# Optimization experiments

Measured on AMD Instinct MI355X. Metric: run time of the kernel, lower is better.

Reference implementation:

```python
import jax, jax.numpy as jnp
import numpy as np

N = 2048; C_IN = 2; H = 32; EMB = 16; OUT = 1; HORIZON = 12
B = 32; T = 16

def setup_inputs() -> dict:
    key = jax.random.key(0)
    ks = jax.random.split(key, 10)
    s = 0.05
    return {
        "x":  jax.random.normal(ks[0], (B, T, N, C_IN), dtype=jnp.float32),
        "E1": jax.random.normal(ks[1], (N, EMB), dtype=jnp.float32) * 0.1,
        "E2": jax.random.normal(ks[2], (N, EMB), dtype=jnp.float32) * 0.1,
        "Wx": jax.random.normal(ks[3], (C_IN, 4 * H), dtype=jnp.float32) * s,
        "bx": jnp.zeros((4 * H,), dtype=jnp.float32),
        "Wh": jax.random.normal(ks[4], (H, 4 * H), dtype=jnp.float32) * s,
        "bh": jnp.zeros((4 * H,), dtype=jnp.float32),
        "Wp": jax.random.normal(ks[5], (H, OUT * HORIZON), dtype=jnp.float32) * s,
        "bp": jnp.zeros((OUT * HORIZON,), dtype=jnp.float32),
    }

def reference(x, E1, E2, Wx, bx, Wh, bh, Wp, bp):
    Bb, Tt, Nn, _ = x.shape
    # adaptive adjacency: softmax(relu(E1 @ E2^T)) over last dim  [N,N]
    A = jax.nn.softmax(jax.nn.relu(E1 @ E2.T), axis=-1)

    def step(carry, xt):
        h, c = carry  # [B,N,H]
        # fused graph-conv gates: (A @ xt) Wx + (A @ h) Wh + biases -> [B,N,4H]
        gates = (jnp.einsum('ij,bjc->bic', A, xt) @ Wx + bx
                 + jnp.einsum('ij,bjh->bih', A, h) @ Wh + bh)
        i, f, o, g = jnp.split(gates, 4, axis=-1)
        i = jax.nn.sigmoid(i); f = jax.nn.sigmoid(f); o = jax.nn.sigmoid(o)
        g = jnp.tanh(g)
        c_t = f * c + i * g
        h_t = o * jnp.tanh(c_t)
        return (h_t, c_t), None

    h0 = jnp.zeros((Bb, Nn, H), dtype=x.dtype)
    c0 = jnp.zeros((Bb, Nn, H), dtype=x.dtype)
    (h_last, _), _ = jax.lax.scan(step, (h0, c0), jnp.transpose(x, (1, 0, 2, 3)))
    out = h_last @ Wp + bp                      # [B,N,horizon*out]
    out = out.reshape(Bb, Nn, HORIZON, OUT)
    return jnp.transpose(out, (0, 2, 1, 3))     # [B,horizon,N,out]
```

## Files before the change

### kernel.cpp

```cpp
#include <hip/hip_runtime.h>
#include <hip/hip_bf16.h>
#include <cstddef>
#include <cstdint>

#define NN 2048
#define CIN 2
#define HH 32
#define EMB 16
#define HOR 12
#define BB 32
#define TT 16
#define GC 128
#define XCOLS 1024
#define HCOLS 1024

#define ATILE_STRIDE 65536
#define BTILE_STRIDE 32768
#define LOPLANE 2097152

typedef __attribute__((ext_vector_type(8))) _Float16 f16x8;
typedef __attribute__((ext_vector_type(16))) float f32x16;

__device__ __forceinline__ void load_lds16(const void* g, void* l) {
    __builtin_amdgcn_global_load_lds(
        (const __attribute__((address_space(1))) void*)g,
        (__attribute__((address_space(3))) void*)l, 16, 0, 0);
}

__global__ __launch_bounds__(256) void e2_transpose(const float* __restrict__ E2,
                                                    float* __restrict__ E2T) {
    const int idx = blockIdx.x * 256 + threadIdx.x;
    const int k = idx >> 11;
    const int j = idx & 2047;
    E2T[idx] = E2[j * EMB + k];
}

__global__ __launch_bounds__(256) void precompute(const float* __restrict__ E1,
                                                  const float* __restrict__ E2T,
                                                  const float* __restrict__ x,
                                                  const float* __restrict__ Wx,
                                                  const float* __restrict__ bx,
                                                  const float* __restrict__ Wh,
                                                  const float* __restrict__ bh,
                                                  _Float16* __restrict__ A2,
                                                  _Float16* __restrict__ B2x,
                                                  _Float16* __restrict__ W16,
                                                  float* __restrict__ Wxr,
                                                  float* __restrict__ bfold) {
    const int blk = blockIdx.x;
    const int tid = threadIdx.x;

    if (blk < 512) {
        const int i = blk * 4 + (tid >> 6);
        const int l = tid & 63;
        float e1[EMB];
#pragma unroll
        for (int k = 0; k < EMB; ++k) e1[k] = E1[i * EMB + k];

        float s[32];
#pragma unroll
        for (int c = 0; c < 32; ++c) s[c] = 0.f;
#pragma unroll
        for (int k = 0; k < EMB; ++k) {
            const float ek = e1[k];
            const float* p = E2T + k * 2048 + l;
#pragma unroll
            for (int c = 0; c < 32; ++c) s[c] = fmaf(ek, p[c * 64], s[c]);
        }
        float mx = 0.f;
#pragma unroll
        for (int c = 0; c < 32; ++c) { s[c] = fmaxf(s[c], 0.f); mx = fmaxf(mx, s[c]); }
#pragma unroll
        for (int off = 32; off > 0; off >>= 1) mx = fmaxf(mx, __shfl_xor(mx, off, 64));
        float sum = 0.f;
#pragma unroll
        for (int c = 0; c < 32; ++c) { s[c] = expf(s[c] - mx); sum += s[c]; }
#pragma unroll
        for (int off = 32; off > 0; off >>= 1) sum += __shfl_xor(sum, off, 64);
        const float inv = 1.0f / sum;
        const int chb = (l >> 3);
        const int e   = l & 7;
#pragma unroll
        for (int c = 0; c < 32; ++c)
            A2[((size_t)(c * 8 + chb) * 2048 + i) * 8 + e] = (_Float16)(s[c] * inv);
    } else if (blk < 512 + 1024) {
        const int idx = (blk - 512) * 256 + tid;
        const int col = idx & 1023;
        const int jc  = idx >> 10;
        const int bt  = col >> 1;
        const int c   = col & 1;
        const float* xp = x + ((size_t)bt * NN + jc * 8) * CIN + c;
        f16x8 vh, vl;
#pragma unroll
        for (int e = 0; e < 8; ++e) {
            const float v = xp[e * CIN];
            const _Float16 hi = (_Float16)v;
            vh[e] = hi;
            vl[e] = (_Float16)(v - (float)hi);
        }
        const size_t base = ((size_t)jc * 1024 + col) * 8;
        *(f16x8*)(B2x + base) = vh;
        *(f16x8*)(B2x + base + LOPLANE) = vl;
    } else {
#pragma unroll
        for (int r = 0; r < 32; ++r) {
            const int idx = r * 256 + tid;
            const int e  = idx & 7;
            const int ln = (idx >> 3) & 63;
            const int gq = (idx >> 9) & 3;
            const int kh = (idx >> 11) & 1;
            const int k  = kh * 16 + (ln >> 5) * 8 + e;
            const int ch = gq * 32 + (ln & 31);
            const float v = Wh[k * GC + (ch & 3) * HH + (ch >> 2)];
            const _Float16 hi = (_Float16)v;
            W16[idx] = hi;
            W16[8192 + idx] = (_Float16)(v - (float)hi);
        }
        {
            const int idx = tid;
            const int c = idx >> 7, rem = idx & 127;
            const int h = rem >> 2, g = rem & 3;
            Wxr[idx] = Wx[c * GC + g * HH + h];
        }
        if (tid < 128) {
            const int h = tid >> 2, g = tid & 3;
            bfold[tid] = bx[g * HH + h] + bh[g * HH + h];
        }
    }
}

template <int NPROD, int GATE>
__global__ __launch_bounds__(512, 2) void gemm_fused(const _Float16* __restrict__ A2,
                                                     const _Float16* __restrict__ B2,
                                                     float* __restrict__ Cout,
                                                     const float* __restrict__ AX,
                                                     const _Float16* __restrict__ W16,
                                                     const float* __restrict__ Wxr,
                                                     const float* __restrict__ bfold,
                                                     float* __restrict__ cst,
                                                     float* __restrict__ h32,
                                                     _Float16* __restrict__ hTout,
                                                     int t, int last) {
    constexpr int SUBS   = (NPROD == 1) ? 2 : 1;
    constexpr int NT     = 64 / SUBS;
    constexpr int SUBBUF = 4096 + NPROD * 8192;
    constexpr int BUF    = SUBS * SUBBUF;
    constexpr int NBUF   = (NPROD == 1) ? 4 : 6;
    constexpr int PCH    = 256 + NPROD * 512;
    constexpr int NG     = (SUBS * PCH) / 64;
    constexpr int GMAX   = 3;
    constexpr int STAGE_SZ = NBUF * BUF;
    constexpr int SMEMSZ = GATE ? (STAGE_SZ + 1024 + 512 + 2048) : STAGE_SZ;
    __shared__ __align__(16) char smem[SMEMSZ];

    const int tid  = threadIdx.x;
    const int w    = tid >> 6;
    const int lane = tid & 63;

    const int wg = blockIdx.x;
    const int x8 = wg & 7;
    const int s  = wg >> 3;
    const int mb = (x8 >> 1) * 8 + (s & 7);
    const int nb = (x8 & 1) * 4 + (s >> 3);
    const int m0 = mb * 64;
    const int n0 = nb * 128;

    float* wxr_s = nullptr; float* bfl_s = nullptr; float* axs = nullptr;
    if constexpr (GATE) {
        wxr_s = (float*)(smem + STAGE_SZ);
        bfl_s = (float*)(smem + STAGE_SZ + 1024);
        axs   = (float*)(smem + STAGE_SZ + 1536);
        const int b0c = nb * 4;
        if (tid < 64) *(float4*)&wxr_s[tid * 4] = *(const float4*)&Wxr[tid * 4];
        if (tid < 32) *(float4*)&bfl_s[tid * 4] = *(const float4*)&bfold[tid * 4];
        axs[tid] = AX[(size_t)(m0 + (tid & 63)) * XCOLS +
                      ((b0c + (tid >> 7)) * TT + t) * CIN + ((tid >> 6) & 1)];
    }

    const _Float16* gp[GMAX];
    int lbase[GMAX];
    int adv[GMAX];
    bool val[GMAX];
#pragma unroll
    for (int i = 0; i < GMAX; ++i) {
        const int g = w + 8 * i;
        val[i] = (g < NG);
        const int gg = val[i] ? g : 0;
        const int cid  = gg * 64 + lane;
        const int cid0 = gg * 64;
        const int su  = cid / PCH,  r  = cid  - su * PCH;
        const int su0 = cid0 / PCH, r0 = cid0 - su0 * PCH;
        if (r < 256) {
            gp[i]  = A2 + ((size_t)((su * 4 + (r >> 6)) * 2048) + m0 + (r & 63)) * 8;
            adv[i] = SUBS * ATILE_STRIDE;
        } else {
            const int r2 = r - 256;
            gp[i]  = B2 + (size_t)(r2 >> 9) * LOPLANE
                        + ((size_t)((su * 4 + ((r2 & 511) >> 7)) * 1024) + n0 + (r2 & 127)) * 8;
            adv[i] = SUBS * BTILE_STRIDE;
        }
        lbase[i] = su0 * SUBBUF + (r0 < 256 ? r0 * 16 : 4096 + (r0 - 256) * 16);
    }

    const int lrow = lane & 31, lg = lane >> 5;
    const int mi = w >> 2;
    const int gq = w & 3;
    const int wc = gq * 32;
    const int aoff0 = lg * 1024 + (mi * 32 + lrow) * 16;
    const int aoff1 = 2048 + lg * 1024 + (mi * 32 + lrow) * 16;
    const int boff0 = 4096 + lg * 2048 + (wc + lrow) * 16;
    const int boff1 = 4096 + 4096 + lg * 2048 + (wc + lrow) * 16;

    f32x16 acc0 = (f32x16)(0.0f), acc1 = (f32x16)(0.0f);

#define STAGE(BUFI) do {                                                       \
    char* lb = smem + (BUFI) * BUF;                                            \
    _Pragma("unroll")                                                          \
    for (int i = 0; i < GMAX; ++i) if (val[i]) {                               \
        load_lds16(gp[i], lb + lbase[i]);                                      \
        gp[i] += adv[i];                                                       \
    }                                                                          \
} while (0)

#define VMW(NHI, NLO) do {                                                     \
    if (w < 4) asm volatile("s_waitcnt vmcnt(" #NHI ")" ::: "memory");         \
    else       asm volatile("s_waitcnt vmcnt(" #NLO ")" ::: "memory");         \
} while (0)

#define BAR() do {                                                             \
    __builtin_amdgcn_s_barrier();                                              \
    asm volatile("" ::: "memory");                                             \
} while (0)

#define COMPUTE(BUFI) do {                                                     \
    const char* sb = smem + (BUFI) * BUF;                                      \
    _Pragma("unroll")                                                          \
    for (int su = 0; su < SUBS; ++su) {                                        \
        const char* st = sb + su * SUBBUF;                                     \
        f16x8 fa0 = *(const f16x8*)(st + aoff0);                               \
        f16x8 fa1 = *(const f16x8*)(st + aoff1);                               \
        f16x8 fb0 = *(const f16x8*)(st + boff0);                               \
        f16x8 fb1 = *(const f16x8*)(st + boff1);                               \
        acc0 = __builtin_amdgcn_mfma_f32_32x32x16_f16(fa0, fb0, acc0, 0, 0, 0);\
        acc1 = __builtin_amdgcn_mfma_f32_32x32x16_f16(fa1, fb1, acc1, 0, 0, 0);\
        if constexpr (NPROD == 2) {                                            \
            f16x8 fc0 = *(const f16x8*)(st + boff0 + 8192);                    \
            f16x8 fc1 = *(const f16x8*)(st + boff1 + 8192);                    \
            acc0 = __builtin_amdgcn_mfma_f32_32x32x16_f16(fa0, fc0, acc0, 0, 0, 0); \
            acc1 = __builtin_amdgcn_mfma_f32_32x32x16_f16(fa1, fc1, acc1, 0, 0, 0); \
        }                                                                      \
    }                                                                          \
} while (0)

    if constexpr (NPROD == 1) {
        STAGE(0);
        STAGE(1);
#pragma unroll 1
        for (int it = 0; it < NT - 2; ++it) {
            STAGE((it + 2) & 3);
            asm volatile("s_waitcnt vmcnt(6)" ::: "memory");
            BAR();
            COMPUTE(it & 3);
        }
        asm volatile("s_waitcnt vmcnt(3)" ::: "memory");
        BAR();
        COMPUTE((NT - 2) & 3);
        asm volatile("s_waitcnt vmcnt(0)" ::: "memory");
        BAR();
        COMPUTE((NT - 1) & 3);
    } else {
        STAGE(0);
        STAGE(1);
        STAGE(2);
        int bs = 3, bc = 0;
#pragma unroll 1
        for (int it = 0; it < NT - 3; ++it) {
            STAGE(bs);
            VMW(9, 6);
            BAR();
            COMPUTE(bc);
            bs = (bs == 5) ? 0 : bs + 1;
            bc = (bc == 5) ? 0 : bc + 1;
        }
        VMW(6, 4);
        BAR();
        COMPUTE(bc); bc = (bc == 5) ? 0 : bc + 1;
        VMW(3, 2);
        BAR();
        COMPUTE(bc); bc = (bc == 5) ? 0 : bc + 1;
        asm volatile("s_waitcnt vmcnt(0)" ::: "memory");
        BAR();
        COMPUTE(bc);
    }
#undef STAGE
#undef VMW
#undef BAR
#undef COMPUTE

    if constexpr (!GATE) {
        const int colg = n0 + wc + lrow;
#pragma unroll
        for (int r = 0; r < 16; ++r) {
            const int rp = (r & 3) + 8 * (r >> 2) + 4 * lg;
            Cout[(size_t)(m0 + mi * 32 + rp) * XCOLS + colg] = acc0[r] + acc1[r];
        }
    } else {
        f16x8 wbh0 = *(const f16x8*)(W16 + ((size_t)(0 * 4 + gq) * 64 + lane) * 8);
        f16x8 wbh1 = *(const f16x8*)(W16 + ((size_t)(1 * 4 + gq) * 64 + lane) * 8);
        f16x8 wbl0 = *(const f16x8*)(W16 + 8192 + ((size_t)(0 * 4 + gq) * 64 + lane) * 8);
        f16x8 wbl1 = *(const f16x8*)(W16 + 8192 + ((size_t)(1 * 4 + gq) * 64 + lane) * 8);

        _Float16* ahh = (_Float16*)smem;
        _Float16* ahl = (_Float16*)(smem + 17408);
        const int colw = wc + lrow;
#pragma unroll
        for (int r = 0; r < 16; ++r) {
            const int rp = (r & 3) + 8 * (r >> 2) + 4 * lg;
            const float v = acc0[r] + acc1[r];
            const _Float16 hi = (_Float16)v;
            ahh[(mi * 32 + rp) * 136 + colw] = hi;
            ahl[(mi * 32 + rp) * 136 + colw] = (_Float16)(v - (float)hi);
        }
        __syncthreads();

        f32x16 g0 = (f32x16)(0.0f), g1 = (f32x16)(0.0f);
        f32x16 g2 = (f32x16)(0.0f), g3 = (f32x16)(0.0f);
#define GATEB(ACC, b) do {                                                         \
    const int arow = (mi * 32 + lrow) * 136 + (b) * 32 + lg * 8;                   \
    f16x8 fh0 = *(const f16x8*)(ahh + arow);                                       \
    f16x8 fl0 = *(const f16x8*)(ahl + arow);                                       \
    f16x8 fh1 = *(const f16x8*)(ahh + arow + 16);                                  \
    f16x8 fl1 = *(const f16x8*)(ahl + arow + 16);                                  \
    ACC = __builtin_amdgcn_mfma_f32_32x32x16_f16(fh0, wbh0, ACC, 0, 0, 0);         \
    ACC = __builtin_amdgcn_mfma_f32_32x32x16_f16(fh0, wbl0, ACC, 0, 0, 0);         \
    ACC = __builtin_amdgcn_mfma_f32_32x32x16_f16(fl0, wbh0, ACC, 0, 0, 0);         \
    ACC = __builtin_amdgcn_mfma_f32_32x32x16_f16(fh1, wbh1, ACC, 0, 0, 0);         \
    ACC = __builtin_amdgcn_mfma_f32_32x32x16_f16(fh1, wbl1, ACC, 0, 0, 0);         \
    ACC = __builtin_amdgcn_mfma_f32_32x32x16_f16(fl1, wbh1, ACC, 0, 0, 0);         \
} while (0)
        GATEB(g0, 0); GATEB(g1, 1); GATEB(g2, 2); GATEB(g3, 3);
#undef GATEB

        float* gl = (float*)(smem + 34816);
        const int nl2 = tid & 63;
        const int hb  = (tid >> 6) * 4;
        const int b0c = nb * 4;
        const int nd  = m0 + nl2;
        const size_t ntbase = ((size_t)((nd >> 5) * 4 + ((nd >> 3) & 3)) * 1024) * 8 + (nd & 7);

#define POINT(ACC, bi) do {                                                        \
    _Pragma("unroll")                                                              \
    for (int r = 0; r < 16; ++r) {                                                 \
        const int rp = (r & 3) + 8 * (r >> 2) + 4 * lg;                            \
        gl[(mi * 32 + rp) * 132 + gq * 32 + lrow] = ACC[r];                        \
    }                                                                              \
    __syncthreads();                                                               \
    {                                                                              \
        const float ax0 = axs[(bi) * 128 + nl2];                                   \
        const float ax1 = axs[(bi) * 128 + 64 + nl2];                              \
        const int bb = b0c + (bi);                                                 \
        const size_t off = (size_t)nd * HCOLS + bb * HH + hb;                      \
        const float4 co = *(const float4*)(cst + off);                             \
        const float cold[4] = {co.x, co.y, co.z, co.w};                            \
        float cn[4], hn[4];                                                        \
        _Pragma("unroll")                                                          \
        for (int p = 0; p < 4; ++p) {                                              \
            const int hh = hb + p;                                                 \
            const float4 gt = *(const float4*)(gl + nl2 * 132 + hh * 4);           \
            const float a0 = gt.x + bfl_s[hh*4+0] + ax0*wxr_s[hh*4+0] + ax1*wxr_s[128+hh*4+0]; \
            const float a1 = gt.y + bfl_s[hh*4+1] + ax0*wxr_s[hh*4+1] + ax1*wxr_s[128+hh*4+1]; \
            const float a2 = gt.z + bfl_s[hh*4+2] + ax0*wxr_s[hh*4+2] + ax1*wxr_s[128+hh*4+2]; \
            const float a3 = gt.w + bfl_s[hh*4+3] + ax0*wxr_s[hh*4+3] + ax1*wxr_s[128+hh*4+3]; \
            const float i_ = 1.0f / (1.0f + expf(-a0));                            \
            const float f_ = 1.0f / (1.0f + expf(-a1));                            \
            const float o_ = 1.0f / (1.0f + expf(-a2));                            \
            const float g_ = tanhf(a3);                                            \
            const float ct = f_ * cold[p] + i_ * g_;                               \
            cn[p] = ct;                                                            \
            hn[p] = o_ * tanhf(ct);                                                \
        }                                                                          \
        *(float4*)(cst + off) = make_float4(cn[0], cn[1], cn[2], cn[3]);           \
        if (last) *(float4*)(h32 + off) = make_float4(hn[0], hn[1], hn[2], hn[3]); \
        _Pragma("unroll")                                                          \
        for (int p = 0; p < 4; ++p)                                                \
            hTout[ntbase + (size_t)(bb * HH + hb + p) * 8] = (_Float16)hn[p];      \
    }                                                                              \
    __syncthreads();                                                               \
} while (0)
        POINT(g0, 0); POINT(g1, 1); POINT(g2, 2); POINT(g3, 3);
#undef POINT
    }
}

__global__ __launch_bounds__(256) void gate_update(const float* __restrict__ AX,
                                                   const float* __restrict__ Wxr,
                                                   const float* __restrict__ bfold,
                                                   float* __restrict__ c,
                                                   float* __restrict__ h32,
                                                   _Float16* __restrict__ hT) {
    const int n0 = blockIdx.x * 64;
    const int b0 = blockIdx.y * 4;
    const int tid = threadIdx.x;
    __shared__ float wxr[256];
    __shared__ float bfl[128];
    __shared__ float axs[2][64];

    if (tid < 64)  *(float4*)&wxr[tid * 4] = *(const float4*)&Wxr[tid * 4];
    if (tid < 32)  *(float4*)&bfl[tid * 4] = *(const float4*)&bfold[tid * 4];

    const int nl = tid & 63;
    const int hq = tid >> 6;

    const int nd = n0 + nl;
    const size_t ntbase = ((size_t)((nd >> 5) * 4 + ((nd >> 3) & 3)) * 1024) * 8 + (nd & 7);

#pragma unroll 1
    for (int bi = 0; bi < 4; ++bi) {
        const int b = b0 + bi;
        if (bi) __syncthreads();
        if (tid < 128) {
            const int which = tid >> 6, nls = tid & 63;
            axs[which][nls] = AX[(size_t)(n0 + nls) * XCOLS + (b * TT + 0) * CIN + which];
        }
        __syncthreads();

        const float ax0 = axs[0][nl], ax1 = axs[1][nl];
        float cn[8], hn[8];
#pragma unroll
        for (int u = 0; u < 8; ++u) {
            const int h = hq * 8 + u;
            float a0 = bfl[h * 4 + 0] + ax0 * wxr[h * 4 + 0] + ax1 * wxr[128 + h * 4 + 0];
            float a1 = bfl[h * 4 + 1] + ax0 * wxr[h * 4 + 1] + ax1 * wxr[128 + h * 4 + 1];
            float a2 = bfl[h * 4 + 2] + ax0 * wxr[h * 4 + 2] + ax1 * wxr[128 + h * 4 + 2];
            float a3 = bfl[h * 4 + 3] + ax0 * wxr[h * 4 + 3] + ax1 * wxr[128 + h * 4 + 3];
            const float i_ = 1.0f / (1.0f + expf(-a0));
            const float f_ = 1.0f / (1.0f + expf(-a1));
            const float o_ = 1.0f / (1.0f + expf(-a2));
            const float g_ = tanhf(a3);
            const float ct = i_ * g_;
            (void)f_;
            cn[u] = ct;
            hn[u] = o_ * tanhf(ct);
        }
        const size_t off = (size_t)nd * HCOLS + b * HH + hq * 8;
        *(float4*)(c + off)       = make_float4(cn[0], cn[1], cn[2], cn[3]);
        *(float4*)(c + off + 4)   = make_float4(cn[4], cn[5], cn[6], cn[7]);
        *(float4*)(h32 + off)     = make_float4(hn[0], hn[1], hn[2], hn[3]);
        *(float4*)(h32 + off + 4) = make_float4(hn[4], hn[5], hn[6], hn[7]);
#pragma unroll
        for (int u = 0; u < 8; ++u)
            hT[ntbase + (size_t)(b * HH + hq * 8 + u) * 8] = (_Float16)hn[u];
    }
}

__global__ __launch_bounds__(256) void head_kernel(const float* __restrict__ h,
                                                   const float* __restrict__ Wp,
                                                   const float* __restrict__ bp,
                                                   float* __restrict__ out) {
    const int idx = blockIdx.x * 256 + threadIdx.x;
    const int b = idx >> 11;
    const int n = idx & (NN - 1);
    float hv[HH];
    const float* hp = h + (size_t)n * HCOLS + b * HH;
#pragma unroll
    for (int k = 0; k < HH; ++k) hv[k] = hp[k];
#pragma unroll
    for (int th = 0; th < HOR; ++th) {
        float acc = bp[th];
#pragma unroll
        for (int k = 0; k < HH; ++k) acc += hv[k] * Wp[k * HOR + th];
        out[((size_t)b * HOR + th) * NN + n] = acc;
    }
}

extern "C" void kernel_launch(void* const* d_in, const int* in_sizes, int n_in,
                              void* d_out, int out_size, void* d_ws, size_t ws_size,
                              hipStream_t stream) {
    const float* x  = (const float*)d_in[0];
    const float* E1 = (const float*)d_in[1];
    const float* E2 = (const float*)d_in[2];
    const float* Wx = (const float*)d_in[3];
    const float* bx = (const float*)d_in[4];
    const float* Wh = (const float*)d_in[5];
    const float* bh = (const float*)d_in[6];
    const float* Wp = (const float*)d_in[7];
    const float* bp = (const float*)d_in[8];

    char* ws = (char*)d_ws;
    _Float16* A2  = (_Float16*)(ws);
    _Float16* B2x = (_Float16*)(ws + ( 8ull << 20));
    _Float16* hT0 = (_Float16*)(ws + (16ull << 20));
    _Float16* hT1 = (_Float16*)(ws + (20ull << 20));
    float* AX   = (float*)(ws + (24ull << 20));
    float* cst  = (float*)(ws + (32ull << 20));
    float* h32  = (float*)(ws + (40ull << 20));
    float* Wxr  = (float*)(ws + (48ull << 20) + 65536);
    float* bfold= (float*)(ws + (48ull << 20) + 131072);
    _Float16* W16 = (_Float16*)(ws + (48ull << 20) + 262144);
    float* E2T  = (float*)(ws + (48ull << 20) + 524288);
    _Float16* hTb[2] = {hT0, hT1};

    e2_transpose<<<128, 256, 0, stream>>>(E2, E2T);

    precompute<<<512 + 1024 + 1, 256, 0, stream>>>(E1, E2T, x, Wx, bx, Wh, bh,
                                                   A2, B2x, W16, Wxr, bfold);

    gemm_fused<2, 0><<<256, 512, 0, stream>>>(A2, B2x, AX, nullptr, nullptr, nullptr,
                                              nullptr, nullptr, nullptr, nullptr, 0, 0);

    gate_update<<<dim3(NN / 64, BB / 4), 256, 0, stream>>>(AX, Wxr, bfold,
                                                           cst, h32, hTb[0]);
    for (int t = 1; t < TT; ++t) {
        gemm_fused<1, 1><<<256, 512, 0, stream>>>(A2, hTb[(t + 1) & 1], nullptr, AX,
                                                  W16, Wxr, bfold, cst, h32,
                                                  hTb[t & 1], t, t == TT - 1 ? 1 : 0);
    }

    head_kernel<<<(BB * NN) / 256, 256, 0, stream>>>(h32, Wp, bp, (float*)d_out);
}
```

Measured before the change: 531.1 us.

## Split K across two wave groups in 1024-thread gemm_fused with LDS reduction

Doubles the workgroup to 1024 threads. The two groups of 8 waves each compute half of the K work: one sub-buffer in the recurrent GEMM, one B plane in the input GEMM. The partial accumulators are then reduced through LDS. The gate epilogue is also split so each half handles two of the four batch gates, and the staging loads and waitcnt thresholds are adjusted to match. This aims to raise wave-level parallelism and MFMA throughput per CU, at the cost of an extra LDS reduction, extra barriers and occupancy limited to one workgroup per CU.

```diff
diff --git a/kernel.cpp b/kernel.cpp
--- a/kernel.cpp
+++ b/kernel.cpp
@@ -130,17 +130,17 @@
 }
 
 template <int NPROD, int GATE>
-__global__ __launch_bounds__(512, 2) void gemm_fused(const _Float16* __restrict__ A2,
-                                                     const _Float16* __restrict__ B2,
-                                                     float* __restrict__ Cout,
-                                                     const float* __restrict__ AX,
-                                                     const _Float16* __restrict__ W16,
-                                                     const float* __restrict__ Wxr,
-                                                     const float* __restrict__ bfold,
-                                                     float* __restrict__ cst,
-                                                     float* __restrict__ h32,
-                                                     _Float16* __restrict__ hTout,
-                                                     int t, int last) {
+__global__ __launch_bounds__(1024, 1) void gemm_fused(const _Float16* __restrict__ A2,
+                                                      const _Float16* __restrict__ B2,
+                                                      float* __restrict__ Cout,
+                                                      const float* __restrict__ AX,
+                                                      const _Float16* __restrict__ W16,
+                                                      const float* __restrict__ Wxr,
+                                                      const float* __restrict__ bfold,
+                                                      float* __restrict__ cst,
+                                                      float* __restrict__ h32,
+                                                      _Float16* __restrict__ hTout,
+                                                      int t, int last) {
     constexpr int SUBS   = (NPROD == 1) ? 2 : 1;
     constexpr int NT     = 64 / SUBS;
     constexpr int SUBBUF = 4096 + NPROD * 8192;
@@ -148,14 +148,17 @@
     constexpr int NBUF   = (NPROD == 1) ? 4 : 6;
     constexpr int PCH    = 256 + NPROD * 512;
     constexpr int NG     = (SUBS * PCH) / 64;
-    constexpr int GMAX   = 3;
+    constexpr int GMAX   = 2;
     constexpr int STAGE_SZ = NBUF * BUF;
-    constexpr int SMEMSZ = GATE ? (STAGE_SZ + 1024 + 512 + 2048) : STAGE_SZ;
+    constexpr int REDOFF = (NPROD == 1) ? 34816 : 86016;
+    constexpr int SMEMSZ = GATE ? 105984 : STAGE_SZ;
     __shared__ __align__(16) char smem[SMEMSZ];
 
     const int tid  = threadIdx.x;
     const int w    = tid >> 6;
     const int lane = tid & 63;
+    const int ws   = w & 7;
+    const int kv   = w >> 3;
 
     const int wg = blockIdx.x;
     const int x8 = wg & 7;
@@ -167,14 +170,15 @@
 
     float* wxr_s = nullptr; float* bfl_s = nullptr; float* axs = nullptr;
     if constexpr (GATE) {
-        wxr_s = (float*)(smem + STAGE_SZ);
-        bfl_s = (float*)(smem + STAGE_SZ + 1024);
-        axs   = (float*)(smem + STAGE_SZ + 1536);
+        wxr_s = (float*)(smem + 102400);
+        bfl_s = (float*)(smem + 103424);
+        axs   = (float*)(smem + 103936);
         const int b0c = nb * 4;
         if (tid < 64) *(float4*)&wxr_s[tid * 4] = *(const float4*)&Wxr[tid * 4];
-        if (tid < 32) *(float4*)&bfl_s[tid * 4] = *(const float4*)&bfold[tid * 4];
-        axs[tid] = AX[(size_t)(m0 + (tid & 63)) * XCOLS +
-                      ((b0c + (tid >> 7)) * TT + t) * CIN + ((tid >> 6) & 1)];
+        if (tid >= 64 && tid < 96) *(float4*)&bfl_s[(tid - 64) * 4] = *(const float4*)&bfold[(tid - 64) * 4];
+        if (tid < 512)
+            axs[tid] = AX[(size_t)(m0 + (tid & 63)) * XCOLS +
+                          ((b0c + (tid >> 7)) * TT + t) * CIN + ((tid >> 6) & 1)];
     }
 
     const _Float16* gp[GMAX];
@@ -183,7 +187,7 @@
     bool val[GMAX];
 #pragma unroll
     for (int i = 0; i < GMAX; ++i) {
-        const int g = w + 8 * i;
+        const int g = w + 16 * i;
         val[i] = (g < NG);
         const int gg = val[i] ? g : 0;
         const int cid  = gg * 64 + lane;
@@ -203,13 +207,15 @@
     }
 
     const int lrow = lane & 31, lg = lane >> 5;
-    const int mi = w >> 2;
-    const int gq = w & 3;
+    const int mi = ws >> 2;
+    const int gq = ws & 3;
     const int wc = gq * 32;
-    const int aoff0 = lg * 1024 + (mi * 32 + lrow) * 16;
-    const int aoff1 = 2048 + lg * 1024 + (mi * 32 + lrow) * 16;
-    const int boff0 = 4096 + lg * 2048 + (wc + lrow) * 16;
-    const int boff1 = 4096 + 4096 + lg * 2048 + (wc + lrow) * 16;
+    const int subbase = (NPROD == 1) ? kv * SUBBUF : 0;
+    const int aoff0 = subbase + lg * 1024 + (mi * 32 + lrow) * 16;
+    const int aoff1 = subbase + 2048 + lg * 1024 + (mi * 32 + lrow) * 16;
+    const int bplane = (NPROD == 2) ? kv * 8192 : 0;
+    const int boff0 = subbase + 4096 + bplane + lg * 2048 + (wc + lrow) * 16;
+    const int boff1 = subbase + 4096 + bplane + 4096 + lg * 2048 + (wc + lrow) * 16;
 
     f32x16 acc0 = (f32x16)(0.0f), acc1 = (f32x16)(0.0f);
 
@@ -222,9 +228,9 @@
     }                                                                          \
 } while (0)
 
-#define VMW(NHI, NLO) do {                                                     \
-    if (w < 4) asm volatile("s_waitcnt vmcnt(" #NHI ")" ::: "memory");         \
-    else       asm volatile("s_waitcnt vmcnt(" #NLO ")" ::: "memory");         \
+#define VMW(PRED, NHI, NLO) do {                                               \
+    if (PRED) asm volatile("s_waitcnt vmcnt(" #NHI ")" ::: "memory");          \
+    else      asm volatile("s_waitcnt vmcnt(" #NLO ")" ::: "memory");          \
 } while (0)
 
 #define BAR() do {                                                             \
@@ -233,23 +239,13 @@
 } while (0)
 
 #define COMPUTE(BUFI) do {                                                     \
-    const char* sb = smem + (BUFI) * BUF;                                      \
-    _Pragma("unroll")                                                          \
-    for (int su = 0; su < SUBS; ++su) {                                        \
-        const char* st = sb + su * SUBBUF;                                     \
-        f16x8 fa0 = *(const f16x8*)(st + aoff0);                               \
-        f16x8 fa1 = *(const f16x8*)(st + aoff1);                               \
-        f16x8 fb0 = *(const f16x8*)(st + boff0);                               \
-        f16x8 fb1 = *(const f16x8*)(st + boff1);                               \
-        acc0 = __builtin_amdgcn_mfma_f32_32x32x16_f16(fa0, fb0, acc0, 0, 0, 0);\
-        acc1 = __builtin_amdgcn_mfma_f32_32x32x16_f16(fa1, fb1, acc1, 0, 0, 0);\
-        if constexpr (NPROD == 2) {                                            \
-            f16x8 fc0 = *(const f16x8*)(st + boff0 + 8192);                    \
-            f16x8 fc1 = *(const f16x8*)(st + boff1 + 8192);                    \
-            acc0 = __builtin_amdgcn_mfma_f32_32x32x16_f16(fa0, fc0, acc0, 0, 0, 0); \
-            acc1 = __builtin_amdgcn_mfma_f32_32x32x16_f16(fa1, fc1, acc1, 0, 0, 0); \
-        }                                                                      \
-    }                                                                          \
+    const char* st = smem + (BUFI) * BUF;                                      \
+    f16x8 fa0 = *(const f16x8*)(st + aoff0);                                   \
+    f16x8 fa1 = *(const f16x8*)(st + aoff1);                                   \
+    f16x8 fb0 = *(const f16x8*)(st + boff0);                                   \
+    f16x8 fb1 = *(const f16x8*)(st + boff1);                                   \
+    acc0 = __builtin_amdgcn_mfma_f32_32x32x16_f16(fa0, fb0, acc0, 0, 0, 0);    \
+    acc1 = __builtin_amdgcn_mfma_f32_32x32x16_f16(fa1, fb1, acc1, 0, 0, 0);    \
 } while (0)
 
     if constexpr (NPROD == 1) {
@@ -258,11 +254,11 @@
 #pragma unroll 1
         for (int it = 0; it < NT - 2; ++it) {
             STAGE((it + 2) & 3);
-            asm volatile("s_waitcnt vmcnt(6)" ::: "memory");
+            VMW(w < 8, 4, 2);
             BAR();
             COMPUTE(it & 3);
         }
-        asm volatile("s_waitcnt vmcnt(3)" ::: "memory");
+        VMW(w < 8, 2, 1);
         BAR();
         COMPUTE((NT - 2) & 3);
         asm volatile("s_waitcnt vmcnt(0)" ::: "memory");
@@ -276,16 +272,16 @@
 #pragma unroll 1
         for (int it = 0; it < NT - 3; ++it) {
             STAGE(bs);
-            VMW(9, 6);
+            VMW(w < 4, 6, 3);
             BAR();
             COMPUTE(bc);
             bs = (bs == 5) ? 0 : bs + 1;
             bc = (bc == 5) ? 0 : bc + 1;
         }
-        VMW(6, 4);
+        VMW(w < 4, 4, 2);
         BAR();
         COMPUTE(bc); bc = (bc == 5) ? 0 : bc + 1;
-        VMW(3, 2);
+        VMW(w < 4, 2, 1);
         BAR();
         COMPUTE(bc); bc = (bc == 5) ? 0 : bc + 1;
         asm volatile("s_waitcnt vmcnt(0)" ::: "memory");
@@ -297,12 +293,32 @@
 #undef BAR
 #undef COMPUTE
 
+    f32x16 fin;
+#pragma unroll
+    for (int r = 0; r < 16; ++r) fin[r] = acc0[r] + acc1[r];
+    {
+        float* red = (float*)(smem + REDOFF);
+        if (kv == 1) {
+            float* rp = red + ws * 1024 + lane;
+#pragma unroll
+            for (int r = 0; r < 16; ++r) rp[r * 64] = fin[r];
+        }
+        __syncthreads();
+        if (kv == 0) {
+            const float* rp = red + ws * 1024 + lane;
+#pragma unroll
+            for (int r = 0; r < 16; ++r) fin[r] += rp[r * 64];
+        }
+    }
+
     if constexpr (!GATE) {
-        const int colg = n0 + wc + lrow;
-#pragma unroll
-        for (int r = 0; r < 16; ++r) {
-            const int rp = (r & 3) + 8 * (r >> 2) + 4 * lg;
-            Cout[(size_t)(m0 + mi * 32 + rp) * XCOLS + colg] = acc0[r] + acc1[r];
+        if (kv == 0) {
+            const int colg = n0 + wc + lrow;
+#pragma unroll
+            for (int r = 0; r < 16; ++r) {
+                const int rp = (r & 3) + 8 * (r >> 2) + 4 * lg;
+                Cout[(size_t)(m0 + mi * 32 + rp) * XCOLS + colg] = fin[r];
+            }
         }
     } else {
         f16x8 wbh0 = *(const f16x8*)(W16 + ((size_t)(0 * 4 + gq) * 64 + lane) * 8);
@@ -312,19 +328,20 @@
 
         _Float16* ahh = (_Float16*)smem;
         _Float16* ahl = (_Float16*)(smem + 17408);
-        const int colw = wc + lrow;
-#pragma unroll
-        for (int r = 0; r < 16; ++r) {
-            const int rp = (r & 3) + 8 * (r >> 2) + 4 * lg;
-            const float v = acc0[r] + acc1[r];
-            const _Float16 hi = (_Float16)v;
-            ahh[(mi * 32 + rp) * 136 + colw] = hi;
-            ahl[(mi * 32 + rp) * 136 + colw] = (_Float16)(v - (float)hi);
+        if (kv == 0) {
+            const int colw = wc + lrow;
+#pragma unroll
+            for (int r = 0; r < 16; ++r) {
+                const int rp = (r & 3) + 8 * (r >> 2) + 4 * lg;
+                const float v = fin[r];
+                const _Float16 hi = (_Float16)v;
+                ahh[(mi * 32 + rp) * 136 + colw] = hi;
+                ahl[(mi * 32 + rp) * 136 + colw] = (_Float16)(v - (float)hi);
+            }
         }
         __syncthreads();
 
         f32x16 g0 = (f32x16)(0.0f), g1 = (f32x16)(0.0f);
-        f32x16 g2 = (f32x16)(0.0f), g3 = (f32x16)(0.0f);
 #define GATEB(ACC, b) do {                                                         \
     const int arow = (mi * 32 + lrow) * 136 + (b) * 32 + lg * 8;                   \
     f16x8 fh0 = *(const f16x8*)(ahh + arow);                                       \
@@ -338,27 +355,32 @@
     ACC = __builtin_amdgcn_mfma_f32_32x32x16_f16(fh1, wbl1, ACC, 0, 0, 0);         \
     ACC = __builtin_amdgcn_mfma_f32_32x32x16_f16(fl1, wbh1, ACC, 0, 0, 0);         \
 } while (0)
-        GATEB(g0, 0); GATEB(g1, 1); GATEB(g2, 2); GATEB(g3, 3);
+        GATEB(g0, kv * 2 + 0);
+        GATEB(g1, kv * 2 + 1);
 #undef GATEB
 
-        float* gl = (float*)(smem + 34816);
-        const int nl2 = tid & 63;
-        const int hb  = (tid >> 6) * 4;
+        float* glk = (float*)(smem + 34816 + kv * 33792);
+        const int kvt  = tid >> 9;
+        const int tid2 = tid & 511;
+        float* glt = (float*)(smem + 34816 + kvt * 33792);
+        const int nl2 = tid2 & 63;
+        const int hb  = (tid2 >> 6) * 4;
         const int b0c = nb * 4;
         const int nd  = m0 + nl2;
         const size_t ntbase = ((size_t)((nd >> 5) * 4 + ((nd >> 3) & 3)) * 1024) * 8 + (nd & 7);
 
-#define POINT(ACC, bi) do {                                                        \
+#define POINTR(GACC, R) do {                                                       \
     _Pragma("unroll")                                                              \
     for (int r = 0; r < 16; ++r) {                                                 \
         const int rp = (r & 3) + 8 * (r >> 2) + 4 * lg;                            \
-        gl[(mi * 32 + rp) * 132 + gq * 32 + lrow] = ACC[r];                        \
+        glk[(mi * 32 + rp) * 132 + gq * 32 + lrow] = GACC[r];                      \
     }                                                                              \
     __syncthreads();                                                               \
     {                                                                              \
-        const float ax0 = axs[(bi) * 128 + nl2];                                   \
-        const float ax1 = axs[(bi) * 128 + 64 + nl2];                              \
-        const int bb = b0c + (bi);                                                 \
+        const int bl  = kvt * 2 + (R);                       \
+        const float ax0 = axs[bl * 128 + nl2];                                     \
+        const float ax1 = axs[bl * 128 + 64 + nl2];                                \
+        const int bb = b0c + bl;                                                   \
         const size_t off = (size_t)nd * HCOLS + bb * HH + hb;                      \
         const float4 co = *(const float4*)(cst + off);                             \
         const float cold[4] = {co.x, co.y, co.z, co.w};                            \
@@ -366,7 +388,7 @@
         _Pragma("unroll")                                                          \
         for (int p = 0; p < 4; ++p) {                                              \
             const int hh = hb + p;                                                 \
-            const float4 gt = *(const float4*)(gl + nl2 * 132 + hh * 4);           \
+            const float4 gt = *(const float4*)(glt + nl2 * 132 + hh * 4);          \
             const float a0 = gt.x + bfl_s[hh*4+0] + ax0*wxr_s[hh*4+0] + ax1*wxr_s[128+hh*4+0]; \
             const float a1 = gt.y + bfl_s[hh*4+1] + ax0*wxr_s[hh*4+1] + ax1*wxr_s[128+hh*4+1]; \
             const float a2 = gt.z + bfl_s[hh*4+2] + ax0*wxr_s[hh*4+2] + ax1*wxr_s[128+hh*4+2]; \
@@ -387,8 +409,9 @@
     }                                                                              \
     __syncthreads();                                                               \
 } while (0)
-        POINT(g0, 0); POINT(g1, 1); POINT(g2, 2); POINT(g3, 3);
-#undef POINT
+        POINTR(g0, 0);
+        POINTR(g1, 1);
+#undef POINTR
     }
 }
 
@@ -505,15 +528,15 @@
     precompute<<<512 + 1024 + 1, 256, 0, stream>>>(E1, E2T, x, Wx, bx, Wh, bh,
                                                    A2, B2x, W16, Wxr, bfold);
 
-    gemm_fused<2, 0><<<256, 512, 0, stream>>>(A2, B2x, AX, nullptr, nullptr, nullptr,
-                                              nullptr, nullptr, nullptr, nullptr, 0, 0);
+    gemm_fused<2, 0><<<256, 1024, 0, stream>>>(A2, B2x, AX, nullptr, nullptr, nullptr,
+                                               nullptr, nullptr, nullptr, nullptr, 0, 0);
 
     gate_update<<<dim3(NN / 64, BB / 4), 256, 0, stream>>>(AX, Wxr, bfold,
                                                            cst, h32, hTb[0]);
     for (int t = 1; t < TT; ++t) {
-        gemm_fused<1, 1><<<256, 512, 0, stream>>>(A2, hTb[(t + 1) & 1], nullptr, AX,
-                                                  W16, Wxr, bfold, cst, h32,
-                                                  hTb[t & 1], t, t == TT - 1 ? 1 : 0);
+        gemm_fused<1, 1><<<256, 1024, 0, stream>>>(A2, hTb[(t + 1) & 1], nullptr, AX,
+                                                   W16, Wxr, bfold, cst, h32,
+                                                   hTb[t & 1], t, t == TT - 1 ? 1 : 0);
     }
 
     head_kernel<<<(BB * NN) / 256, 256, 0, stream>>>(h32, Wp, bp, (float*)d_out);
```

Result: no change. 533.6 us (+0.5%).

## Split K across wave pairs in single-product GEMM path with LDS reduction

Applied to the files above, without the earlier changes.

For the NPROD==1 path, each wave now covers both 32-row M tiles and handles one K sub-slice, where before each wave covered one M tile and looped over all sub-slices. Partial accumulators from the two K-halves are summed through LDS before the epilogue. Each B fragment load now feeds two MFMAs, which cuts LDS reads per MFMA. The cost is extra accumulator registers, an LDS reduction with two additional barriers, and the epilogue running on only half the waves.

```diff
diff --git a/kernel.cpp b/kernel.cpp
--- a/kernel.cpp
+++ b/kernel.cpp
@@ -210,8 +210,18 @@
     const int aoff1 = 2048 + lg * 1024 + (mi * 32 + lrow) * 16;
     const int boff0 = 4096 + lg * 2048 + (wc + lrow) * 16;
     const int boff1 = 4096 + 4096 + lg * 2048 + (wc + lrow) * 16;
+    const int gqk = w & 3;
+    const int kvk = w >> 2;
+    const int subb  = kvk * SUBBUF;
+    const int a00 = subb + lg * 1024 + lrow * 16;
+    const int a01 = subb + 2048 + lg * 1024 + lrow * 16;
+    const int a10 = a00 + 512;
+    const int a11 = a01 + 512;
+    const int bk0 = subb + 4096 + lg * 2048 + (gqk * 32 + lrow) * 16;
+    const int bk1 = bk0 + 4096;
 
     f32x16 acc0 = (f32x16)(0.0f), acc1 = (f32x16)(0.0f);
+    f32x16 acc2 = (f32x16)(0.0f), acc3 = (f32x16)(0.0f);
 
 #define STAGE(BUFI) do {                                                       \
     char* lb = smem + (BUFI) * BUF;                                            \
@@ -232,24 +242,32 @@
     asm volatile("" ::: "memory");                                             \
 } while (0)
 
-#define COMPUTE(BUFI) do {                                                     \
-    const char* sb = smem + (BUFI) * BUF;                                      \
-    _Pragma("unroll")                                                          \
-    for (int su = 0; su < SUBS; ++su) {                                        \
-        const char* st = sb + su * SUBBUF;                                     \
-        f16x8 fa0 = *(const f16x8*)(st + aoff0);                               \
-        f16x8 fa1 = *(const f16x8*)(st + aoff1);                               \
-        f16x8 fb0 = *(const f16x8*)(st + boff0);                               \
-        f16x8 fb1 = *(const f16x8*)(st + boff1);                               \
-        acc0 = __builtin_amdgcn_mfma_f32_32x32x16_f16(fa0, fb0, acc0, 0, 0, 0);\
-        acc1 = __builtin_amdgcn_mfma_f32_32x32x16_f16(fa1, fb1, acc1, 0, 0, 0);\
-        if constexpr (NPROD == 2) {                                            \
-            f16x8 fc0 = *(const f16x8*)(st + boff0 + 8192);                    \
-            f16x8 fc1 = *(const f16x8*)(st + boff1 + 8192);                    \
-            acc0 = __builtin_amdgcn_mfma_f32_32x32x16_f16(fa0, fc0, acc0, 0, 0, 0); \
-            acc1 = __builtin_amdgcn_mfma_f32_32x32x16_f16(fa1, fc1, acc1, 0, 0, 0); \
-        }                                                                      \
-    }                                                                          \
+#define COMPUTE1(BUFI) do {                                                    \
+    const char* st = smem + (BUFI) * BUF;                                      \
+    f16x8 fa00 = *(const f16x8*)(st + a00);                                    \
+    f16x8 fa01 = *(const f16x8*)(st + a01);                                    \
+    f16x8 fa10 = *(const f16x8*)(st + a10);                                    \
+    f16x8 fa11 = *(const f16x8*)(st + a11);                                    \
+    f16x8 fb0  = *(const f16x8*)(st + bk0);                                    \
+    f16x8 fb1  = *(const f16x8*)(st + bk1);                                    \
+    acc0 = __builtin_amdgcn_mfma_f32_32x32x16_f16(fa00, fb0, acc0, 0, 0, 0);   \
+    acc1 = __builtin_amdgcn_mfma_f32_32x32x16_f16(fa01, fb1, acc1, 0, 0, 0);   \
+    acc2 = __builtin_amdgcn_mfma_f32_32x32x16_f16(fa10, fb0, acc2, 0, 0, 0);   \
+    acc3 = __builtin_amdgcn_mfma_f32_32x32x16_f16(fa11, fb1, acc3, 0, 0, 0);   \
+} while (0)
+
+#define COMPUTE2(BUFI) do {                                                    \
+    const char* st = smem + (BUFI) * BUF;                                      \
+    f16x8 fa0 = *(const f16x8*)(st + aoff0);                                   \
+    f16x8 fa1 = *(const f16x8*)(st + aoff1);                                   \
+    f16x8 fb0 = *(const f16x8*)(st + boff0);                                   \
+    f16x8 fb1 = *(const f16x8*)(st + boff1);                                   \
+    acc0 = __builtin_amdgcn_mfma_f32_32x32x16_f16(fa0, fb0, acc0, 0, 0, 0);    \
+    acc1 = __builtin_amdgcn_mfma_f32_32x32x16_f16(fa1, fb1, acc1, 0, 0, 0);    \
+    f16x8 fc0 = *(const f16x8*)(st + boff0 + 8192);                            \
+    f16x8 fc1 = *(const f16x8*)(st + boff1 + 8192);                            \
+    acc0 = __builtin_amdgcn_mfma_f32_32x32x16_f16(fa0, fc0, acc0, 0, 0, 0);    \
+    acc1 = __builtin_amdgcn_mfma_f32_32x32x16_f16(fa1, fc1, acc1, 0, 0, 0);    \
 } while (0)
 
     if constexpr (NPROD == 1) {
@@ -260,14 +278,14 @@
             STAGE((it + 2) & 3);
             asm volatile("s_waitcnt vmcnt(6)" ::: "memory");
             BAR();
-            COMPUTE(it & 3);
+            COMPUTE1(it & 3);
         }
         asm volatile("s_waitcnt vmcnt(3)" ::: "memory");
         BAR();
-        COMPUTE((NT - 2) & 3);
+        COMPUTE1((NT - 2) & 3);
         asm volatile("s_waitcnt vmcnt(0)" ::: "memory");
         BAR();
-        COMPUTE((NT - 1) & 3);
+        COMPUTE1((NT - 1) & 3);
     } else {
         STAGE(0);
         STAGE(1);
@@ -278,53 +296,85 @@
             STAGE(bs);
             VMW(9, 6);
             BAR();
-            COMPUTE(bc);
+            COMPUTE2(bc);
             bs = (bs == 5) ? 0 : bs + 1;
             bc = (bc == 5) ? 0 : bc + 1;
         }
         VMW(6, 4);
         BAR();
-        COMPUTE(bc); bc = (bc == 5) ? 0 : bc + 1;
+        COMPUTE2(bc); bc = (bc == 5) ? 0 : bc + 1;
         VMW(3, 2);
         BAR();
-        COMPUTE(bc); bc = (bc == 5) ? 0 : bc + 1;
+        COMPUTE2(bc); bc = (bc == 5) ? 0 : bc + 1;
         asm volatile("s_waitcnt vmcnt(0)" ::: "memory");
         BAR();
-        COMPUTE(bc);
+        COMPUTE2(bc);
     }
 #undef STAGE
 #undef VMW
 #undef BAR
-#undef COMPUTE
-
-    if constexpr (!GATE) {
-        const int colg = n0 + wc + lrow;
-#pragma unroll
-        for (int r = 0; r < 16; ++r) {
-            const int rp = (r & 3) + 8 * (r >> 2) + 4 * lg;
-            Cout[(size_t)(m0 + mi * 32 + rp) * XCOLS + colg] = acc0[r] + acc1[r];
-        }
-    } else {
-        f16x8 wbh0 = *(const f16x8*)(W16 + ((size_t)(0 * 4 + gq) * 64 + lane) * 8);
-        f16x8 wbh1 = *(const f16x8*)(W16 + ((size_t)(1 * 4 + gq) * 64 + lane) * 8);
-        f16x8 wbl0 = *(const f16x8*)(W16 + 8192 + ((size_t)(0 * 4 + gq) * 64 + lane) * 8);
-        f16x8 wbl1 = *(const f16x8*)(W16 + 8192 + ((size_t)(1 * 4 + gq) * 64 + lane) * 8);
-
-        _Float16* ahh = (_Float16*)smem;
-        _Float16* ahl = (_Float16*)(smem + 17408);
-        const int colw = wc + lrow;
-#pragma unroll
-        for (int r = 0; r < 16; ++r) {
-            const int rp = (r & 3) + 8 * (r >> 2) + 4 * lg;
-            const float v = acc0[r] + acc1[r];
-            const _Float16 hi = (_Float16)v;
-            ahh[(mi * 32 + rp) * 136 + colw] = hi;
-            ahl[(mi * 32 + rp) * 136 + colw] = (_Float16)(v - (float)hi);
-        }
-        __syncthreads();
-
-        f32x16 g0 = (f32x16)(0.0f), g1 = (f32x16)(0.0f);
-        f32x16 g2 = (f32x16)(0.0f), g3 = (f32x16)(0.0f);
+#undef COMPUTE1
+#undef COMPUTE2
+
+    if constexpr (NPROD == 1) {
+        f32x16 fin0, fin1;
+#pragma unroll
+        for (int r = 0; r < 16; ++r) { fin0[r] = acc0[r] + acc1[r]; fin1[r] = acc2[r] + acc3[r]; }
+        {
+            float* red = (float*)smem;
+            if (kvk == 1) {
+                float* rp0 = red + (gqk * 2 + 0) * 1024 + lane;
+                float* rp1 = red + (gqk * 2 + 1) * 1024 + lane;
+#pragma unroll
+                for (int r = 0; r < 16; ++r) { rp0[r * 64] = fin0[r]; rp1[r * 64] = fin1[r]; }
+            }
+            __syncthreads();
+            if (kvk == 0) {
+                const float* rp0 = red + (gqk * 2 + 0) * 1024 + lane;
+                const float* rp1 = red + (gqk * 2 + 1) * 1024 + lane;
+#pragma unroll
+                for (int r = 0; r < 16; ++r) { fin0[r] += rp0[r * 64]; fin1[r] += rp1[r * 64]; }
+            }
+            __syncthreads();
+        }
+
+        if constexpr (!GATE) {
+            if (kvk == 0) {
+                const int colg = n0 + gqk * 32 + lrow;
+#pragma unroll
+                for (int r = 0; r < 16; ++r) {
+                    const int rp = (r & 3) + 8 * (r >> 2) + 4 * lg;
+                    Cout[(size_t)(m0 + rp) * XCOLS + colg]      = fin0[r];
+                    Cout[(size_t)(m0 + 32 + rp) * XCOLS + colg] = fin1[r];
+                }
+            }
+        } else {
+            f16x8 wbh0 = *(const f16x8*)(W16 + ((size_t)(0 * 4 + gq) * 64 + lane) * 8);
+            f16x8 wbh1 = *(const f16x8*)(W16 + ((size_t)(1 * 4 + gq) * 64 + lane) * 8);
+            f16x8 wbl0 = *(const f16x8*)(W16 + 8192 + ((size_t)(0 * 4 + gq) * 64 + lane) * 8);
+            f16x8 wbl1 = *(const f16x8*)(W16 + 8192 + ((size_t)(1 * 4 + gq) * 64 + lane) * 8);
+
+            _Float16* ahh = (_Float16*)smem;
+            _Float16* ahl = (_Float16*)(smem + 17408);
+            if (kvk == 0) {
+                const int colw = gqk * 32 + lrow;
+#pragma unroll
+                for (int r = 0; r < 16; ++r) {
+                    const int rp = (r & 3) + 8 * (r >> 2) + 4 * lg;
+                    const float v0 = fin0[r];
+                    const _Float16 h0 = (_Float16)v0;
+                    ahh[rp * 136 + colw] = h0;
+                    ahl[rp * 136 + colw] = (_Float16)(v0 - (float)h0);
+                    const float v1 = fin1[r];
+                    const _Float16 h1 = (_Float16)v1;
+                    ahh[(32 + rp) * 136 + colw] = h1;
+                    ahl[(32 + rp) * 136 + colw] = (_Float16)(v1 - (float)h1);
+                }
+            }
+            __syncthreads();
+
+            f32x16 g0 = (f32x16)(0.0f), g1 = (f32x16)(0.0f);
+            f32x16 g2 = (f32x16)(0.0f), g3 = (f32x16)(0.0f);
 #define GATEB(ACC, b) do {                                                         \
     const int arow = (mi * 32 + lrow) * 136 + (b) * 32 + lg * 8;                   \
     f16x8 fh0 = *(const f16x8*)(ahh + arow);                                       \
@@ -338,15 +388,15 @@
     ACC = __builtin_amdgcn_mfma_f32_32x32x16_f16(fh1, wbl1, ACC, 0, 0, 0);         \
     ACC = __builtin_amdgcn_mfma_f32_32x32x16_f16(fl1, wbh1, ACC, 0, 0, 0);         \
 } while (0)
-        GATEB(g0, 0); GATEB(g1, 1); GATEB(g2, 2); GATEB(g3, 3);
+            GATEB(g0, 0); GATEB(g1, 1); GATEB(g2, 2); GATEB(g3, 3);
 #undef GATEB
 
-        float* gl = (float*)(smem + 34816);
-        const int nl2 = tid & 63;
-        const int hb  = (tid >> 6) * 4;
-        const int b0c = nb * 4;
-        const int nd  = m0 + nl2;
-        const size_t ntbase = ((size_t)((nd >> 5) * 4 + ((nd >> 3) & 3)) * 1024) * 8 + (nd & 7);
+            float* gl = (float*)(smem + 34816);
+            const int nl2 = tid & 63;
+            const int hb  = (tid >> 6) * 4;
+            const int b0c = nb * 4;
+            const int nd  = m0 + nl2;
+            const size_t ntbase = ((size_t)((nd >> 5) * 4 + ((nd >> 3) & 3)) * 1024) * 8 + (nd & 7);
 
 #define POINT(ACC, bi) do {                                                        \
     _Pragma("unroll")                                                              \
@@ -387,8 +437,16 @@
     }                                                                              \
     __syncthreads();                                                               \
 } while (0)
-        POINT(g0, 0); POINT(g1, 1); POINT(g2, 2); POINT(g3, 3);
+            POINT(g0, 0); POINT(g1, 1); POINT(g2, 2); POINT(g3, 3);
 #undef POINT
+        }
+    } else {
+        const int colg = n0 + wc + lrow;
+#pragma unroll
+        for (int r = 0; r < 16; ++r) {
+            const int rp = (r & 3) + 8 * (r >> 2) + 4 * lg;
+            Cout[(size_t)(m0 + mi * 32 + rp) * XCOLS + colg] = acc0[r] + acc1[r];
+        }
     }
 }
 
```

Measured after the change: 536.6 us (median of 2 runs). Within noise of the previous version (+1.0%).
